# Optimization experiments

Hardware: AMD Instinct MI355X
Metric: run time of the kernel (lower is better)

The kernel has to match this reference:

```python
import jax, jax.numpy as jnp
import numpy as np

L, B, H, S, V, D = 2, 128, 1024, 512, 32000, 64
W_SCALE = 0.02

def setup_inputs() -> dict:
    key = jax.random.key(0)
    ks = jax.random.split(key, 17)
    f = lambda k, shape: jax.random.normal(k, shape, dtype=jnp.float32)
    return {
        "input_ids": jax.random.randint(ks[0], (1, B), 0, V),
        "h": f(ks[1], (L, B, H)),
        "c": f(ks[2], (L, B, H)),
        "h_s": f(ks[3], (S, B, H)),
        "emb": f(ks[4], (V, H)),
        "W_pt": f(ks[5], (H, H)) * W_SCALE,
        "b_pt": f(ks[6], (H,)) * W_SCALE,
        "v_pt": f(ks[7], (H,)) * W_SCALE,
        "b_v": f(ks[8], (1,)) * W_SCALE,
        "W_a": f(ks[9], (H, H)) * W_SCALE,
        "b_a": f(ks[10], (1,)) * W_SCALE,
        "W_ih": f(ks[11], (L, 4 * H, H)) * W_SCALE,
        "W_hh": f(ks[12], (L, 4 * H, H)) * W_SCALE,
        "b_ih": f(ks[13], (L, 4 * H)) * W_SCALE,
        "b_hh": f(ks[14], (L, 4 * H)) * W_SCALE,
        "W_out": f(ks[15], (V, H)) * W_SCALE,
        "b_out": f(ks[16], (V,)) * W_SCALE,
    }


def reference(input_ids, h, c, h_s, emb, W_pt, b_pt, v_pt, b_v, W_a, b_a,
              W_ih, W_hh, b_ih, b_hh, W_out, b_out):
    S_len = h_s.shape[0]
    x_emb = emb[input_ids]                     # [1, B, H]
    h_top = h[-1]                              # [B, H] top-layer decoder state
    # predicted alignment position p_t = S * sigmoid(v . tanh(W h + b))
    p_t = S_len * jax.nn.sigmoid(jnp.tanh(h_top @ W_pt.T + b_pt) @ v_pt + b_v[0])  # [B]
    s = jnp.clip(jnp.round(p_t).astype(jnp.int32), D, S_len - 1 - D)               # [B]
    # gather local window h_s[s-D : s+D+1] per batch element
    idx = s[:, None] + jnp.arange(-D, D + 1)    # [B, 2D+1]
    h_s_b = jnp.transpose(h_s, (1, 0, 2))       # [B, S, H]
    h_loc = jnp.take_along_axis(h_s_b, idx[:, :, None], axis=1)  # [B, 2D+1, H]
    # bilinear score h_t^T W_a h_s_j per window position
    scores = jnp.einsum('bh,hk,bjk->bj', h_top, W_a, h_loc) + b_a[0]  # [B, 2D+1]
    sigma2 = (D / 2.0) ** 2
    gauss = jnp.exp(-((idx.astype(p_t.dtype) - p_t[:, None]) ** 2) / (2.0 * sigma2))
    a_t = jax.nn.softmax(scores, axis=-1) * gauss                      # [B, 2D+1]
    context = jnp.einsum('bj,bjh->bh', a_t, h_loc)                     # [B, H]
    # inject context into the LSTM hidden state, then run one step
    h_in = h + context[None]                    # [L, B, H]
    x = x_emb[0]                                # [B, H]
    hs, cs = [], []
    for l in range(h.shape[0]):
        gates = x @ W_ih[l].T + b_ih[l] + h_in[l] @ W_hh[l].T + b_hh[l]
        i, f, g, o = jnp.split(gates, 4, axis=-1)
        c_new = jax.nn.sigmoid(f) * c[l] + jax.nn.sigmoid(i) * jnp.tanh(g)
        h_new = jax.nn.sigmoid(o) * jnp.tanh(c_new)
        hs.append(h_new)
        cs.append(c_new)
        x = h_new
    h_out = jnp.stack(hs)                       # [L, B, H]
    c_out = jnp.stack(cs)                       # [L, B, H]
    logits = jax.nn.log_softmax(x @ W_out.T + b_out, axis=-1)  # [B, V]
    return logits, h_out, c_out, context, s
```

## Files before the change

kernel.cpp:

```cpp
#include <hip/hip_runtime.h>
#include <hip/hip_bf16.h>
#include <math.h>

typedef __bf16 bf16_8 __attribute__((ext_vector_type(8)));
typedef __bf16 bf16_4 __attribute__((ext_vector_type(4)));
typedef float  f32x4  __attribute__((ext_vector_type(4)));

static __device__ __forceinline__ float sigmoidf_(float x){ return 1.0f/(1.0f + expf(-x)); }

#define BB 128
#define HH 1024
#define SS 512
#define VV 32000

#define OFF_A0    0u
#define OFF_A1    524288u
#define OFF_ALOG  1048576u
#define OFF_AH    1310720u
#define OFF_AM    1572864u
#define OFF_AL    1835008u
#define OFF_WAT   2097152u
#define OFF_Q     6291456u
#define OFF_Z     6815744u
#define OFF_PT    7340032u
#define OFF_SI    7340544u
#define OFF_SC    7341056u
#define OFF_AT    7408640u
#define OFF_G0    7476224u
#define OFF_G1    9573376u
#define OFF_PMAX  11670528u
#define OFF_PSUM  11801600u
#define OFF_LSE   11932672u

__global__ void k_transpose(const float* __restrict__ in, float* __restrict__ out){
  __shared__ float t[32][33];
  int kt = blockIdx.x, nt = blockIdx.y;
  int c = threadIdx.x & 31, r0 = threadIdx.x >> 5;
  #pragma unroll
  for (int i = 0; i < 4; ++i){
    int r = r0 + 8*i;
    t[r][c] = in[(size_t)(kt*32 + r)*HH + nt*32 + c];
  }
  __syncthreads();
  #pragma unroll
  for (int i = 0; i < 4; ++i){
    int r = r0 + 8*i;
    out[(size_t)(nt*32 + r)*HH + kt*32 + c] = t[c][r];
  }
}

__global__ void k_prep(const int* __restrict__ ids, const float* __restrict__ emb,
                       const float* __restrict__ h,
                       const float* __restrict__ b_pt,
                       const float* __restrict__ b_ih, const float* __restrict__ b_hh,
                       __bf16* __restrict__ A0, __bf16* __restrict__ Ah,
                       __bf16* __restrict__ Am, __bf16* __restrict__ Al,
                       float* __restrict__ z, float* __restrict__ q,
                       float* __restrict__ g0, float* __restrict__ g1){
  int blk = blockIdx.x, t = threadIdx.x;
  if (blk < BB){
    int b = blk, c = t*4;
    int tok = ids[b];
    f32x4 e = *(const f32x4*)(emb + (size_t)tok*HH + c);
    bf16_4 e4;
    #pragma unroll
    for (int i=0;i<4;i++) e4[i] = (__bf16)e[i];
    *(bf16_4*)(A0 + (size_t)b*2048 + c) = e4;
    f32x4 x = *(const f32x4*)(h + (size_t)BB*HH + (size_t)b*HH + c);
    bf16_4 hi4, mi4, lo4;
    #pragma unroll
    for (int i=0;i<4;i++){
      float v = x[i];
      __bf16 bh = (__bf16)v; float r1 = v - (float)bh;
      __bf16 bm = (__bf16)r1; float r2 = r1 - (float)bm;
      hi4[i]=bh; mi4[i]=bm; lo4[i]=(__bf16)r2;
    }
    *(bf16_4*)(Ah + (size_t)b*HH + c) = hi4;
    *(bf16_4*)(Am + (size_t)b*HH + c) = mi4;
    *(bf16_4*)(Al + (size_t)b*HH + c) = lo4;
    *(f32x4*)(z + (size_t)b*HH + c) = *(const f32x4*)(b_pt + c);
    *(f32x4*)(q + (size_t)b*HH + c) = f32x4{0.f,0.f,0.f,0.f};
  } else {
    int b = blk - BB;
    for (int i=t; i<4096; i+=256){
      g0[(size_t)b*4096 + i] = b_ih[i] + b_hh[i];
      g1[(size_t)b*4096 + i] = b_ih[4096+i] + b_hh[4096+i];
    }
  }
}

template<int PREC, int EPI>
__global__ __launch_bounds__(256) void k_gemm(
    const __bf16* __restrict__ Ah, const __bf16* __restrict__ Am, const __bf16* __restrict__ Al,
    int lda,
    const float* __restrict__ B1, const float* __restrict__ B2, int K1, int K2,
    const float* __restrict__ bias,
    float* __restrict__ C, int N,
    float* __restrict__ Pmax, float* __restrict__ Psum)
{
  constexpr int NS  = PREC;
  constexpr int BK  = (PREC == 1) ? 64 : 32;
  constexpr int KG  = BK/8;
  constexpr int TILE = 128*BK*2;
  constexpr int UPT = (128*KG)/256;
  __shared__ __align__(16) char smem[NS*2*TILE];
  char* sA = smem;
  char* sB = smem + NS*TILE;

  const int t = threadIdx.x;
  const int lane = t & 63, wave = t >> 6;
  const int wm = wave >> 1, wn = wave & 1;
  const int quad = lane >> 4, ln = lane & 15;
  const int nblock = blockIdx.x * 128;
  const int K = K1 + K2;
  const int kchunk = K / gridDim.y;
  const int kstart = blockIdx.y * kchunk;
  const int kend = kstart + kchunk;

  f32x4 acc[4][4];
  #pragma unroll
  for (int i=0;i<4;i++)
    #pragma unroll
    for (int j=0;j<4;j++) acc[i][j] = f32x4{0.f,0.f,0.f,0.f};

  if constexpr (PREC == 1){
    uint4 aR[UPT]; f32x4 bR[UPT][2];
    auto issue = [&](int k0){
      #pragma unroll
      for (int i=0;i<UPT;++i){
        int u = t + 256*i, row = u/KG, kg = u%KG;
        aR[i] = *(const uint4*)(Ah + (size_t)row*lda + k0 + kg*8);
        int ng = nblock + row;
        const float* src = (k0 < K1) ? (B1 + (size_t)ng*K1 + k0 + kg*8)
                                     : (B2 + (size_t)ng*K2 + (k0 - K1) + kg*8);
        bR[i][0] = *(const f32x4*)(src);
        bR[i][1] = *(const f32x4*)(src + 4);
      }
    };
    issue(kstart);
    for (int k0 = kstart; k0 < kend; k0 += BK){
      __syncthreads();
      #pragma unroll
      for (int i=0;i<UPT;++i){
        int u = t + 256*i, row = u/KG, kg = u%KG;
        int sl = row*(BK*2) + (((kg ^ (row & (KG-1)))) << 4);
        *(uint4*)(sA + sl) = aR[i];
        bf16_8 hi;
        #pragma unroll
        for (int q=0;q<8;++q) hi[q] = (__bf16)((q<4) ? bR[i][0][q] : bR[i][1][q-4]);
        *(bf16_8*)(sB + sl) = hi;
      }
      __syncthreads();
      if (k0 + BK < kend) issue(k0 + BK);
      #pragma unroll
      for (int ks = 0; ks < BK/32; ++ks){
        bf16_8 af[4], bfr[4];
        #pragma unroll
        for (int mt=0; mt<4; ++mt){
          int row = wm*64 + mt*16 + ln;
          int kg = ks*4 + quad;
          int sl = row*(BK*2) + (((kg ^ (row & (KG-1)))) << 4);
          af[mt] = *(const bf16_8*)(sA + sl);
        }
        #pragma unroll
        for (int nt=0; nt<4; ++nt){
          int row = wn*64 + nt*16 + ln;
          int kg = ks*4 + quad;
          int sl = row*(BK*2) + (((kg ^ (row & (KG-1)))) << 4);
          bfr[nt] = *(const bf16_8*)(sB + sl);
        }
        #pragma unroll
        for (int mt=0; mt<4; ++mt)
          #pragma unroll
          for (int nt=0; nt<4; ++nt)
            acc[mt][nt] = __builtin_amdgcn_mfma_f32_16x16x32_bf16(af[mt], bfr[nt], acc[mt][nt], 0,0,0);
      }
    }
  } else {
    for (int k0 = kstart; k0 < kend; k0 += BK){
      #pragma unroll
      for (int i = 0; i < UPT; ++i){
        int u = t + 256*i;
        int row = u / KG, kg = u % KG;
        int sl = row*(BK*2) + (((kg ^ (row & (KG-1)))) << 4);
        *(uint4*)(sA + sl) = *(const uint4*)(Ah + (size_t)row*lda + k0 + kg*8);
        if constexpr (PREC >= 2)
          *(uint4*)(sA + TILE + sl) = *(const uint4*)(Am + (size_t)row*lda + k0 + kg*8);
        if constexpr (PREC >= 3)
          *(uint4*)(sA + 2*TILE + sl) = *(const uint4*)(Al + (size_t)row*lda + k0 + kg*8);
        int ng = nblock + row;
        const float* src = B1 + (size_t)ng*K1 + k0 + kg*8;
        f32x4 x0 = *(const f32x4*)(src);
        f32x4 x1 = *(const f32x4*)(src + 4);
        bf16_8 hi, mi, lo;
        #pragma unroll
        for (int q=0;q<8;q++){
          float v = (q<4) ? x0[q] : x1[q-4];
          __bf16 bh = (__bf16)v;
          hi[q] = bh;
          float r1 = v - (float)bh;
          __bf16 bm = (__bf16)r1;
          mi[q] = bm;
          lo[q] = (__bf16)(r1 - (float)bm);
        }
        *(bf16_8*)(sB + sl) = hi;
        if constexpr (PREC >= 2) *(bf16_8*)(sB + TILE + sl) = mi;
        if constexpr (PREC >= 3) *(bf16_8*)(sB + 2*TILE + sl) = lo;
      }
      __syncthreads();
      #pragma unroll
      for (int ks = 0; ks < BK/32; ++ks){
        bf16_8 af[NS][4], bfr[NS][4];
        #pragma unroll
        for (int mt=0; mt<4; ++mt){
          int row = wm*64 + mt*16 + ln;
          int kg = ks*4 + quad;
          int sl = row*(BK*2) + (((kg ^ (row & (KG-1)))) << 4);
          #pragma unroll
          for (int s=0;s<NS;s++) af[s][mt] = *(const bf16_8*)(sA + s*TILE + sl);
        }
        #pragma unroll
        for (int nt=0; nt<4; ++nt){
          int row = wn*64 + nt*16 + ln;
          int kg = ks*4 + quad;
          int sl = row*(BK*2) + (((kg ^ (row & (KG-1)))) << 4);
          #pragma unroll
          for (int s=0;s<NS;s++) bfr[s][nt] = *(const bf16_8*)(sB + s*TILE + sl);
        }
        #pragma unroll
        for (int mt=0; mt<4; ++mt)
          #pragma unroll
          for (int nt=0; nt<4; ++nt){
            acc[mt][nt] = __builtin_amdgcn_mfma_f32_16x16x32_bf16(af[0][mt], bfr[0][nt], acc[mt][nt], 0,0,0);
            if constexpr (PREC >= 2){
              acc[mt][nt] = __builtin_amdgcn_mfma_f32_16x16x32_bf16(af[0][mt], bfr[1][nt], acc[mt][nt], 0,0,0);
              acc[mt][nt] = __builtin_amdgcn_mfma_f32_16x16x32_bf16(af[1][mt], bfr[0][nt], acc[mt][nt], 0,0,0);
            }
            if constexpr (PREC >= 3){
              acc[mt][nt] = __builtin_amdgcn_mfma_f32_16x16x32_bf16(af[0][mt], bfr[2][nt], acc[mt][nt], 0,0,0);
              acc[mt][nt] = __builtin_amdgcn_mfma_f32_16x16x32_bf16(af[1][mt], bfr[1][nt], acc[mt][nt], 0,0,0);
              acc[mt][nt] = __builtin_amdgcn_mfma_f32_16x16x32_bf16(af[2][mt], bfr[0][nt], acc[mt][nt], 0,0,0);
            }
          }
      }
      __syncthreads();
    }
  }

  if constexpr (EPI == 0){
    #pragma unroll
    for (int nt=0; nt<4; ++nt){
      int n = nblock + wn*64 + nt*16 + ln;
      float bv = bias ? bias[n] : 0.f;
      #pragma unroll
      for (int mt=0; mt<4; ++mt){
        int m0 = wm*64 + mt*16 + quad*4;
        #pragma unroll
        for (int r=0;r<4;++r)
          C[(size_t)(m0 + r)*N + n] = acc[mt][nt][r] + bv;
      }
    }
  } else if constexpr (EPI == 3){
    #pragma unroll
    for (int nt=0; nt<4; ++nt){
      int n = nblock + wn*64 + nt*16 + ln;
      #pragma unroll
      for (int mt=0; mt<4; ++mt){
        int m0 = wm*64 + mt*16 + quad*4;
        #pragma unroll
        for (int r=0;r<4;++r)
          atomicAdd(C + (size_t)(m0 + r)*N + n, acc[mt][nt][r]);
      }
    }
  } else if constexpr (EPI == 2){
    __syncthreads();
    float* redm = (float*)smem;
    float* reds = (float*)smem + 256;
    float rmax[16];
    #pragma unroll
    for (int mt=0; mt<4; ++mt)
      #pragma unroll
      for (int r=0;r<4;++r){
        float m4 = -1e30f;
        #pragma unroll
        for (int nt=0;nt<4;++nt){
          int n = nblock + wn*64 + nt*16 + ln;
          m4 = fmaxf(m4, acc[mt][nt][r] + bias[n]);
        }
        #pragma unroll
        for (int m=1;m<16;m<<=1) m4 = fmaxf(m4, __shfl_xor(m4, m));
        rmax[mt*4+r] = m4;
      }
    if (ln == 0){
      #pragma unroll
      for (int mt=0;mt<4;++mt)
        #pragma unroll
        for (int r=0;r<4;++r)
          redm[wn*128 + wm*64 + mt*16 + quad*4 + r] = rmax[mt*4+r];
    }
    __syncthreads();
    #pragma unroll
    for (int mt=0; mt<4; ++mt)
      #pragma unroll
      for (int r=0;r<4;++r){
        int row = wm*64 + mt*16 + quad*4 + r;
        float M = fmaxf(redm[row], redm[128 + row]);
        float s4 = 0.f;
        #pragma unroll
        for (int nt=0;nt<4;++nt){
          int n = nblock + wn*64 + nt*16 + ln;
          float v = acc[mt][nt][r] + bias[n];
          C[(size_t)row*N + n] = v;
          s4 += expf(v - M);
        }
        #pragma unroll
        for (int m=1;m<16;m<<=1) s4 += __shfl_xor(s4, m);
        if (ln == 0) reds[wn*128 + row] = s4;
      }
    __syncthreads();
    if (wn == 0 && ln == 0){
      #pragma unroll
      for (int mt=0;mt<4;++mt)
        #pragma unroll
        for (int r=0;r<4;++r){
          int row = wm*64 + mt*16 + quad*4 + r;
          float M = fmaxf(redm[row], redm[128 + row]);
          Pmax[(size_t)blockIdx.x*128 + row] = M;
          Psum[(size_t)blockIdx.x*128 + row] = reds[row] + reds[128 + row];
        }
    }
  }
}

__global__ void k_s2(const float* __restrict__ z, const float* __restrict__ v_pt,
                     const float* __restrict__ b_v,
                     float* __restrict__ p_t, int* __restrict__ s_i, float* __restrict__ out_s){
  __shared__ float red[4];
  int b = blockIdx.x, t = threadIdx.x;
  f32x4 zv = *(const f32x4*)(z + (size_t)b*HH + t*4);
  f32x4 vv = *(const f32x4*)(v_pt + t*4);
  float s = tanhf(zv[0])*vv[0] + tanhf(zv[1])*vv[1] + tanhf(zv[2])*vv[2] + tanhf(zv[3])*vv[3];
  #pragma unroll
  for (int m=1;m<64;m<<=1) s += __shfl_xor(s, m);
  if ((t&63)==0) red[t>>6] = s;
  __syncthreads();
  if (t == 0){
    float tot = red[0]+red[1]+red[2]+red[3] + b_v[0];
    float p = (float)SS * sigmoidf_(tot);
    float sf = rintf(p);
    sf = fminf(fmaxf(sf, 64.0f), 447.0f);
    p_t[b] = p; s_i[b] = (int)sf; out_s[b] = sf;
  }
}

__global__ void k_scores(const float* __restrict__ q, const float* __restrict__ h_s,
                         const int* __restrict__ s_i, const float* __restrict__ b_a,
                         float* __restrict__ sc){
  int b = blockIdx.x;
  int jj = blockIdx.y*4 + (threadIdx.x >> 6);
  if (jj >= 129) return;
  int lane = threadIdx.x & 63;
  int pos = s_i[b] - 64 + jj;
  const float* row = h_s + ((size_t)pos*BB + b)*HH;
  const float* qb  = q + (size_t)b*HH;
  f32x4 a = f32x4{0.f,0.f,0.f,0.f};
  #pragma unroll
  for (int c = lane*4; c < HH; c += 256){
    f32x4 r4 = *(const f32x4*)(row + c);
    f32x4 q4 = *(const f32x4*)(qb + c);
    a += r4*q4;
  }
  float s = a[0]+a[1]+a[2]+a[3];
  #pragma unroll
  for (int m=1;m<64;m<<=1) s += __shfl_xor(s, m);
  if (lane == 0) sc[b*132 + jj] = s + b_a[0];
}

__global__ void k_softmax(const float* __restrict__ sc, const int* __restrict__ s_i,
                          const float* __restrict__ p_t, float* __restrict__ a_t){
  int b = blockIdx.x, l = threadIdx.x;
  const float* scb = sc + b*132;
  float mx = -1e30f;
  for (int j=l; j<129; j+=64) mx = fmaxf(mx, scb[j]);
  #pragma unroll
  for (int m=1;m<64;m<<=1) mx = fmaxf(mx, __shfl_xor(mx, m));
  float sum = 0.f;
  for (int j=l; j<129; j+=64) sum += expf(scb[j] - mx);
  #pragma unroll
  for (int m=1;m<64;m<<=1) sum += __shfl_xor(sum, m);
  float inv = 1.0f/sum;
  float pt = p_t[b]; float s0 = (float)(s_i[b] - 64);
  for (int j=l; j<129; j+=64){
    float e = expf(scb[j]-mx)*inv;
    float d = (s0 + (float)j) - pt;
    a_t[b*132 + j] = e * expf(-(d*d) * (1.0f/2048.0f));
  }
}

__global__ __launch_bounds__(256) void k_context(
    const float* __restrict__ a_t, const float* __restrict__ h_s,
    const int* __restrict__ s_i, const float* __restrict__ h,
    float* __restrict__ ctx_out, __bf16* __restrict__ A0, __bf16* __restrict__ A1){
  __shared__ float sat[132];
  __shared__ float sctx[4][1024];
  int b = blockIdx.x, t = threadIdx.x;
  int w = t >> 6, l = t & 63;
  if (t < 129) sat[t] = a_t[b*132 + t];
  __syncthreads();
  int pos0 = s_i[b] - 64;
  int jstart = (w == 0) ? 0 : (33 + 32*(w-1));
  int jcnt   = (w == 0) ? 33 : 32;
  const float* base = h_s + ((size_t)pos0*BB + b)*HH;
  f32x4 acc[4];
  #pragma unroll
  for (int qq=0;qq<4;++qq) acc[qq] = f32x4{0.f,0.f,0.f,0.f};
  for (int j = jstart; j < jstart + jcnt; ++j){
    const float* row = base + (size_t)j*BB*HH;
    float aj = sat[j];
    #pragma unroll
    for (int qq=0;qq<4;++qq){
      f32x4 r = *(const f32x4*)(row + qq*256 + l*4);
      acc[qq] += r * aj;
    }
  }
  #pragma unroll
  for (int qq=0;qq<4;++qq)
    *(f32x4*)(&sctx[w][qq*256 + l*4]) = acc[qq];
  __syncthreads();
  int c = t*4;
  f32x4 v = *(f32x4*)(&sctx[0][c]) + *(f32x4*)(&sctx[1][c])
          + *(f32x4*)(&sctx[2][c]) + *(f32x4*)(&sctx[3][c]);
  *(f32x4*)(ctx_out + (size_t)b*HH + c) = v;
  f32x4 h0 = *(const f32x4*)(h + (size_t)b*HH + c) + v;
  f32x4 h1 = *(const f32x4*)(h + (size_t)BB*HH + (size_t)b*HH + c) + v;
  bf16_4 v0, v1;
  #pragma unroll
  for (int i=0;i<4;i++){ v0[i]=(__bf16)h0[i]; v1[i]=(__bf16)h1[i]; }
  *(bf16_4*)(A0 + (size_t)b*2048 + 1024 + c) = v0;
  *(bf16_4*)(A1 + (size_t)b*2048 + 1024 + c) = v1;
}

__global__ void k_cell(const float* __restrict__ gates, const float* __restrict__ c_in,
                       float* __restrict__ h_out, float* __restrict__ c_out,
                       __bf16* __restrict__ Anext, int strideNext){
  int g = blockIdx.x*256 + threadIdx.x;
  int b = g >> 10, hc = g & 1023;
  const float* gb = gates + (size_t)b*4096;
  float ig = gb[hc], fg = gb[1024+hc], gg = gb[2048+hc], og = gb[3072+hc];
  float cn = sigmoidf_(fg)*c_in[g] + sigmoidf_(ig)*tanhf(gg);
  float hn = sigmoidf_(og)*tanhf(cn);
  c_out[g] = cn; h_out[g] = hn;
  Anext[(size_t)b*strideNext + hc] = (__bf16)hn;
}

__global__ void k_lse2(const float* __restrict__ Pmax, const float* __restrict__ Psum,
                       float* __restrict__ lse){
  int b = blockIdx.x, l = threadIdx.x;
  float M = -1e30f;
  for (int i=l; i<250; i+=64) M = fmaxf(M, Pmax[(size_t)i*128 + b]);
  #pragma unroll
  for (int m=1;m<64;m<<=1) M = fmaxf(M, __shfl_xor(M, m));
  float s = 0.f;
  for (int i=l; i<250; i+=64) s += Psum[(size_t)i*128 + b] * expf(Pmax[(size_t)i*128 + b] - M);
  #pragma unroll
  for (int m=1;m<64;m<<=1) s += __shfl_xor(s, m);
  if (l == 0) lse[b] = M + logf(s);
}

__global__ void k_sub(float* __restrict__ out, const float* __restrict__ lse){
  int b = blockIdx.y;
  int i = blockIdx.x*256 + threadIdx.x*4;
  float L = lse[b];
  f32x4 v = *(f32x4*)(out + (size_t)b*VV + i);
  v[0]-=L; v[1]-=L; v[2]-=L; v[3]-=L;
  *(f32x4*)(out + (size_t)b*VV + i) = v;
}

extern "C" void kernel_launch(void* const* d_in, const int* in_sizes, int n_in,
                              void* d_out, int out_size, void* d_ws, size_t ws_size,
                              hipStream_t stream){
  const int*   ids   = (const int*)d_in[0];
  const float* h     = (const float*)d_in[1];
  const float* c     = (const float*)d_in[2];
  const float* h_s   = (const float*)d_in[3];
  const float* emb   = (const float*)d_in[4];
  const float* W_pt  = (const float*)d_in[5];
  const float* b_pt  = (const float*)d_in[6];
  const float* v_pt  = (const float*)d_in[7];
  const float* b_v   = (const float*)d_in[8];
  const float* W_a   = (const float*)d_in[9];
  const float* b_a   = (const float*)d_in[10];
  const float* W_ih  = (const float*)d_in[11];
  const float* W_hh  = (const float*)d_in[12];
  const float* b_ih  = (const float*)d_in[13];
  const float* b_hh  = (const float*)d_in[14];
  const float* W_out = (const float*)d_in[15];
  const float* b_out = (const float*)d_in[16];

  char* ws = (char*)d_ws;
  __bf16* A0   = (__bf16*)(ws + OFF_A0);
  __bf16* A1   = (__bf16*)(ws + OFF_A1);
  __bf16* Alog = (__bf16*)(ws + OFF_ALOG);
  __bf16* Ah   = (__bf16*)(ws + OFF_AH);
  __bf16* Am   = (__bf16*)(ws + OFF_AM);
  __bf16* Al   = (__bf16*)(ws + OFF_AL);
  float* WaT   = (float*)(ws + OFF_WAT);
  float* q     = (float*)(ws + OFF_Q);
  float* z     = (float*)(ws + OFF_Z);
  float* p_t   = (float*)(ws + OFF_PT);
  int*   s_i   = (int*)  (ws + OFF_SI);
  float* sc    = (float*)(ws + OFF_SC);
  float* a_t   = (float*)(ws + OFF_AT);
  float* g0    = (float*)(ws + OFF_G0);
  float* g1    = (float*)(ws + OFF_G1);
  float* Pmax  = (float*)(ws + OFF_PMAX);
  float* Psum  = (float*)(ws + OFF_PSUM);
  float* lse   = (float*)(ws + OFF_LSE);

  float* out        = (float*)d_out;
  float* out_logits = out;
  float* out_h      = out + 4096000;
  float* out_c      = out + 4358144;
  float* out_ctx    = out + 4620288;
  float* out_s      = out + 4751360;

  k_transpose<<<dim3(32,32), 256, 0, stream>>>(W_a, WaT);
  k_prep<<<256, 256, 0, stream>>>(ids, emb, h, b_pt, b_ih, b_hh, A0, Ah, Am, Al, z, q, g0, g1);
  k_gemm<2,3><<<dim3(8,4), 256, 0, stream>>>(Ah, Am, nullptr, 1024, WaT, nullptr, 1024, 0,
                                             nullptr, q, 1024, nullptr, nullptr);
  k_gemm<3,3><<<dim3(8,4), 256, 0, stream>>>(Ah, Am, Al, 1024, W_pt, nullptr, 1024, 0,
                                             nullptr, z, 1024, nullptr, nullptr);
  k_s2<<<128, 256, 0, stream>>>(z, v_pt, b_v, p_t, s_i, out_s);
  k_scores<<<dim3(128, 33), 256, 0, stream>>>(q, h_s, s_i, b_a, sc);
  k_softmax<<<128, 64, 0, stream>>>(sc, s_i, p_t, a_t);
  k_context<<<128, 256, 0, stream>>>(a_t, h_s, s_i, h, out_ctx, A0, A1);
  k_gemm<1,3><<<dim3(32,4), 256, 0, stream>>>(A0, nullptr, nullptr, 2048, W_ih, W_hh, 1024, 1024,
                                              nullptr, g0, 4096, nullptr, nullptr);
  k_cell<<<512, 256, 0, stream>>>(g0, c, out_h, out_c, A1, 2048);
  k_gemm<1,3><<<dim3(32,4), 256, 0, stream>>>(A1, nullptr, nullptr, 2048, W_ih + 4194304, W_hh + 4194304,
                                              1024, 1024, nullptr, g1, 4096, nullptr, nullptr);
  k_cell<<<512, 256, 0, stream>>>(g1, c + 131072, out_h + 131072, out_c + 131072, Alog, 1024);
  k_gemm<1,2><<<dim3(250,1), 256, 0, stream>>>(Alog, nullptr, nullptr, 1024, W_out, nullptr, 1024, 0,
                                               b_out, out_logits, 32000, Pmax, Psum);
  k_lse2<<<128, 64, 0, stream>>>(Pmax, Psum, lse);
  k_sub<<<dim3(125,128), 64, 0, stream>>>(out_logits, lse);
}
```

Before: 653.1 us.

## Fuse attention and LSTM pipeline kernels, replace atomics with split-K partial buffers

Merges the W_a transpose and the prep work into one launch, and runs the q and z small GEMMs together in one kernel. The p_t/s computation moves into the scores kernel, and the softmax plus gaussian weighting moves into the context kernel, which now splits each batch row across two blocks. The LSTM gate GEMMs write split-K partials to separate buffers instead of using atomicAdd; the cell kernel sums the four partials and adds the biases. LSE reduction and subtraction become one kernel. This cuts launch count, bias-init traffic and atomic contention, but adds recomputation of p_t in every score block and of LSE in every subtract block, plus extra partial-buffer traffic.

```diff
diff --git a/kernel.cpp b/kernel.cpp
--- a/kernel.cpp
+++ b/kernel.cpp
@@ -25,41 +25,35 @@
 #define OFF_PT    7340032u
 #define OFF_SI    7340544u
 #define OFF_SC    7341056u
-#define OFF_AT    7408640u
-#define OFF_G0    7476224u
-#define OFF_G1    9573376u
-#define OFF_PMAX  11670528u
-#define OFF_PSUM  11801600u
-#define OFF_LSE   11932672u
-
-__global__ void k_transpose(const float* __restrict__ in, float* __restrict__ out){
-  __shared__ float t[32][33];
-  int kt = blockIdx.x, nt = blockIdx.y;
-  int c = threadIdx.x & 31, r0 = threadIdx.x >> 5;
-  #pragma unroll
-  for (int i = 0; i < 4; ++i){
-    int r = r0 + 8*i;
-    t[r][c] = in[(size_t)(kt*32 + r)*HH + nt*32 + c];
-  }
-  __syncthreads();
-  #pragma unroll
-  for (int i = 0; i < 4; ++i){
-    int r = r0 + 8*i;
-    out[(size_t)(nt*32 + r)*HH + kt*32 + c] = t[c][r];
-  }
-}
-
-__global__ void k_prep(const int* __restrict__ ids, const float* __restrict__ emb,
-                       const float* __restrict__ h,
-                       const float* __restrict__ b_pt,
-                       const float* __restrict__ b_ih, const float* __restrict__ b_hh,
-                       __bf16* __restrict__ A0, __bf16* __restrict__ Ah,
-                       __bf16* __restrict__ Am, __bf16* __restrict__ Al,
-                       float* __restrict__ z, float* __restrict__ q,
-                       float* __restrict__ g0, float* __restrict__ g1){
+#define OFF_G0P   7408640u
+#define OFF_G1P   15797248u
+#define OFF_PMAX  24185856u
+#define OFF_PSUM  24313856u
+
+__global__ void k_prep_all(const float* __restrict__ W_a, float* __restrict__ WaT,
+                           const int* __restrict__ ids, const float* __restrict__ emb,
+                           const float* __restrict__ h, const float* __restrict__ b_pt,
+                           __bf16* __restrict__ A0, __bf16* __restrict__ Ah,
+                           __bf16* __restrict__ Am, __bf16* __restrict__ Al,
+                           float* __restrict__ z, float* __restrict__ q){
+  __shared__ float tsm[32][33];
   int blk = blockIdx.x, t = threadIdx.x;
-  if (blk < BB){
-    int b = blk, c = t*4;
+  if (blk < 1024){
+    int kt = blk & 31, nt = blk >> 5;
+    int c = t & 31, r0 = t >> 5;
+    #pragma unroll
+    for (int i = 0; i < 4; ++i){
+      int r = r0 + 8*i;
+      tsm[r][c] = W_a[(size_t)(kt*32 + r)*HH + nt*32 + c];
+    }
+    __syncthreads();
+    #pragma unroll
+    for (int i = 0; i < 4; ++i){
+      int r = r0 + 8*i;
+      WaT[(size_t)(nt*32 + r)*HH + kt*32 + c] = tsm[c][r];
+    }
+  } else {
+    int b = blk - 1024, c = t*4;
     int tok = ids[b];
     f32x4 e = *(const f32x4*)(emb + (size_t)tok*HH + c);
     bf16_4 e4;
@@ -80,13 +74,130 @@
     *(bf16_4*)(Al + (size_t)b*HH + c) = lo4;
     *(f32x4*)(z + (size_t)b*HH + c) = *(const f32x4*)(b_pt + c);
     *(f32x4*)(q + (size_t)b*HH + c) = f32x4{0.f,0.f,0.f,0.f};
-  } else {
-    int b = blk - BB;
-    for (int i=t; i<4096; i+=256){
-      g0[(size_t)b*4096 + i] = b_ih[i] + b_hh[i];
-      g1[(size_t)b*4096 + i] = b_ih[4096+i] + b_hh[4096+i];
-    }
-  }
+  }
+}
+
+template<int PREC>
+__device__ __forceinline__ void gemm_small(
+    char* smem,
+    const __bf16* __restrict__ Ah, const __bf16* __restrict__ Am, const __bf16* __restrict__ Al,
+    int lda, const float* __restrict__ B1, int K,
+    float* __restrict__ C, int N, int xblk, int ysplit)
+{
+  constexpr int NS   = PREC;
+  constexpr int BK   = 32;
+  constexpr int KG   = BK/8;
+  constexpr int TILE = 128*BK*2;
+  constexpr int UPT  = (128*KG)/256;
+  char* sA = smem;
+  char* sB = smem + NS*TILE;
+
+  const int t = threadIdx.x;
+  const int lane = t & 63, wave = t >> 6;
+  const int wm = wave >> 1, wn = wave & 1;
+  const int quad = lane >> 4, ln = lane & 15;
+  const int nblock = xblk * 128;
+  const int kchunk = K / ysplit;
+  const int kstart = blockIdx.y * kchunk;
+  const int kend = kstart + kchunk;
+
+  f32x4 acc[4][4];
+  #pragma unroll
+  for (int i=0;i<4;i++)
+    #pragma unroll
+    for (int j=0;j<4;j++) acc[i][j] = f32x4{0.f,0.f,0.f,0.f};
+
+  for (int k0 = kstart; k0 < kend; k0 += BK){
+    #pragma unroll
+    for (int i = 0; i < UPT; ++i){
+      int u = t + 256*i;
+      int row = u / KG, kg = u % KG;
+      int sl = row*(BK*2) + (((kg ^ (row & (KG-1)))) << 4);
+      *(uint4*)(sA + sl) = *(const uint4*)(Ah + (size_t)row*lda + k0 + kg*8);
+      if constexpr (PREC >= 2)
+        *(uint4*)(sA + TILE + sl) = *(const uint4*)(Am + (size_t)row*lda + k0 + kg*8);
+      if constexpr (PREC >= 3)
+        *(uint4*)(sA + 2*TILE + sl) = *(const uint4*)(Al + (size_t)row*lda + k0 + kg*8);
+      int ng = nblock + row;
+      const float* src = B1 + (size_t)ng*K + k0 + kg*8;
+      f32x4 x0 = *(const f32x4*)(src);
+      f32x4 x1 = *(const f32x4*)(src + 4);
+      bf16_8 hi, mi, lo;
+      #pragma unroll
+      for (int qv=0;qv<8;qv++){
+        float v = (qv<4) ? x0[qv] : x1[qv-4];
+        __bf16 bh = (__bf16)v;
+        hi[qv] = bh;
+        float r1 = v - (float)bh;
+        __bf16 bm = (__bf16)r1;
+        mi[qv] = bm;
+        lo[qv] = (__bf16)(r1 - (float)bm);
+      }
+      *(bf16_8*)(sB + sl) = hi;
+      if constexpr (PREC >= 2) *(bf16_8*)(sB + TILE + sl) = mi;
+      if constexpr (PREC >= 3) *(bf16_8*)(sB + 2*TILE + sl) = lo;
+    }
+    __syncthreads();
+    {
+      bf16_8 af[NS][4], bfr[NS][4];
+      #pragma unroll
+      for (int mt=0; mt<4; ++mt){
+        int row = wm*64 + mt*16 + ln;
+        int kg = quad;
+        int sl = row*(BK*2) + (((kg ^ (row & (KG-1)))) << 4);
+        #pragma unroll
+        for (int s=0;s<NS;s++) af[s][mt] = *(const bf16_8*)(sA + s*TILE + sl);
+      }
+      #pragma unroll
+      for (int nt=0; nt<4; ++nt){
+        int row = wn*64 + nt*16 + ln;
+        int kg = quad;
+        int sl = row*(BK*2) + (((kg ^ (row & (KG-1)))) << 4);
+        #pragma unroll
+        for (int s=0;s<NS;s++) bfr[s][nt] = *(const bf16_8*)(sB + s*TILE + sl);
+      }
+      #pragma unroll
+      for (int mt=0; mt<4; ++mt)
+        #pragma unroll
+        for (int nt=0; nt<4; ++nt){
+          acc[mt][nt] = __builtin_amdgcn_mfma_f32_16x16x32_bf16(af[0][mt], bfr[0][nt], acc[mt][nt], 0,0,0);
+          if constexpr (PREC >= 2){
+            acc[mt][nt] = __builtin_amdgcn_mfma_f32_16x16x32_bf16(af[0][mt], bfr[1][nt], acc[mt][nt], 0,0,0);
+            acc[mt][nt] = __builtin_amdgcn_mfma_f32_16x16x32_bf16(af[1][mt], bfr[0][nt], acc[mt][nt], 0,0,0);
+          }
+          if constexpr (PREC >= 3){
+            acc[mt][nt] = __builtin_amdgcn_mfma_f32_16x16x32_bf16(af[0][mt], bfr[2][nt], acc[mt][nt], 0,0,0);
+            acc[mt][nt] = __builtin_amdgcn_mfma_f32_16x16x32_bf16(af[1][mt], bfr[1][nt], acc[mt][nt], 0,0,0);
+            acc[mt][nt] = __builtin_amdgcn_mfma_f32_16x16x32_bf16(af[2][mt], bfr[0][nt], acc[mt][nt], 0,0,0);
+          }
+        }
+    }
+    __syncthreads();
+  }
+
+  #pragma unroll
+  for (int nt=0; nt<4; ++nt){
+    int n = nblock + wn*64 + nt*16 + ln;
+    #pragma unroll
+    for (int mt=0; mt<4; ++mt){
+      int m0 = wm*64 + mt*16 + quad*4;
+      #pragma unroll
+      for (int r=0;r<4;++r)
+        atomicAdd(C + (size_t)(m0 + r)*N + n, acc[mt][nt][r]);
+    }
+  }
+}
+
+__global__ __launch_bounds__(256) void k_qz(
+    const __bf16* __restrict__ Ah, const __bf16* __restrict__ Am, const __bf16* __restrict__ Al,
+    const float* __restrict__ WaT, const float* __restrict__ Wpt,
+    float* __restrict__ q, float* __restrict__ z)
+{
+  __shared__ __align__(16) char smem[49152];
+  if (blockIdx.x < 8)
+    gemm_small<2>(smem, Ah, Am, nullptr, 1024, WaT, 1024, q, 1024, blockIdx.x, 4);
+  else
+    gemm_small<3>(smem, Ah, Am, Al, 1024, Wpt, 1024, z, 1024, blockIdx.x - 8, 4);
 }
 
 template<int PREC, int EPI>
@@ -98,14 +209,13 @@
     float* __restrict__ C, int N,
     float* __restrict__ Pmax, float* __restrict__ Psum)
 {
-  constexpr int NS  = PREC;
-  constexpr int BK  = (PREC == 1) ? 64 : 32;
+  constexpr int BK  = 64;
   constexpr int KG  = BK/8;
   constexpr int TILE = 128*BK*2;
   constexpr int UPT = (128*KG)/256;
-  __shared__ __align__(16) char smem[NS*2*TILE];
+  __shared__ __align__(16) char smem[2*TILE];
   char* sA = smem;
-  char* sB = smem + NS*TILE;
+  char* sB = smem + TILE;
 
   const int t = threadIdx.x;
   const int lane = t & 63, wave = t >> 6;
@@ -123,153 +233,70 @@
     #pragma unroll
     for (int j=0;j<4;j++) acc[i][j] = f32x4{0.f,0.f,0.f,0.f};
 
-  if constexpr (PREC == 1){
-    uint4 aR[UPT]; f32x4 bR[UPT][2];
-    auto issue = [&](int k0){
-      #pragma unroll
-      for (int i=0;i<UPT;++i){
-        int u = t + 256*i, row = u/KG, kg = u%KG;
-        aR[i] = *(const uint4*)(Ah + (size_t)row*lda + k0 + kg*8);
-        int ng = nblock + row;
-        const float* src = (k0 < K1) ? (B1 + (size_t)ng*K1 + k0 + kg*8)
-                                     : (B2 + (size_t)ng*K2 + (k0 - K1) + kg*8);
-        bR[i][0] = *(const f32x4*)(src);
-        bR[i][1] = *(const f32x4*)(src + 4);
-      }
-    };
-    issue(kstart);
-    for (int k0 = kstart; k0 < kend; k0 += BK){
-      __syncthreads();
-      #pragma unroll
-      for (int i=0;i<UPT;++i){
-        int u = t + 256*i, row = u/KG, kg = u%KG;
+  uint4 aR[UPT]; f32x4 bR[UPT][2];
+  auto issue = [&](int k0){
+    #pragma unroll
+    for (int i=0;i<UPT;++i){
+      int u = t + 256*i, row = u/KG, kg = u%KG;
+      aR[i] = *(const uint4*)(Ah + (size_t)row*lda + k0 + kg*8);
+      int ng = nblock + row;
+      const float* src = (k0 < K1) ? (B1 + (size_t)ng*K1 + k0 + kg*8)
+                                   : (B2 + (size_t)ng*K2 + (k0 - K1) + kg*8);
+      bR[i][0] = *(const f32x4*)(src);
+      bR[i][1] = *(const f32x4*)(src + 4);
+    }
+  };
+  issue(kstart);
+  for (int k0 = kstart; k0 < kend; k0 += BK){
+    __syncthreads();
+    #pragma unroll
+    for (int i=0;i<UPT;++i){
+      int u = t + 256*i, row = u/KG, kg = u%KG;
+      int sl = row*(BK*2) + (((kg ^ (row & (KG-1)))) << 4);
+      *(uint4*)(sA + sl) = aR[i];
+      bf16_8 hi;
+      #pragma unroll
+      for (int qv=0;qv<8;++qv) hi[qv] = (__bf16)((qv<4) ? bR[i][0][qv] : bR[i][1][qv-4]);
+      *(bf16_8*)(sB + sl) = hi;
+    }
+    __syncthreads();
+    if (k0 + BK < kend) issue(k0 + BK);
+    #pragma unroll
+    for (int ks = 0; ks < BK/32; ++ks){
+      bf16_8 af[4], bfr[4];
+      #pragma unroll
+      for (int mt=0; mt<4; ++mt){
+        int row = wm*64 + mt*16 + ln;
+        int kg = ks*4 + quad;
         int sl = row*(BK*2) + (((kg ^ (row & (KG-1)))) << 4);
-        *(uint4*)(sA + sl) = aR[i];
-        bf16_8 hi;
-        #pragma unroll
-        for (int q=0;q<8;++q) hi[q] = (__bf16)((q<4) ? bR[i][0][q] : bR[i][1][q-4]);
-        *(bf16_8*)(sB + sl) = hi;
-      }
-      __syncthreads();
-      if (k0 + BK < kend) issue(k0 + BK);
-      #pragma unroll
-      for (int ks = 0; ks < BK/32; ++ks){
-        bf16_8 af[4], bfr[4];
-        #pragma unroll
-        for (int mt=0; mt<4; ++mt){
-          int row = wm*64 + mt*16 + ln;
-          int kg = ks*4 + quad;
-          int sl = row*(BK*2) + (((kg ^ (row & (KG-1)))) << 4);
-          af[mt] = *(const bf16_8*)(sA + sl);
-        }
-        #pragma unroll
-        for (int nt=0; nt<4; ++nt){
-          int row = wn*64 + nt*16 + ln;
-          int kg = ks*4 + quad;
-          int sl = row*(BK*2) + (((kg ^ (row & (KG-1)))) << 4);
-          bfr[nt] = *(const bf16_8*)(sB + sl);
-        }
-        #pragma unroll
-        for (int mt=0; mt<4; ++mt)
-          #pragma unroll
-          for (int nt=0; nt<4; ++nt)
-            acc[mt][nt] = __builtin_amdgcn_mfma_f32_16x16x32_bf16(af[mt], bfr[nt], acc[mt][nt], 0,0,0);
-      }
-    }
-  } else {
-    for (int k0 = kstart; k0 < kend; k0 += BK){
-      #pragma unroll
-      for (int i = 0; i < UPT; ++i){
-        int u = t + 256*i;
-        int row = u / KG, kg = u % KG;
+        af[mt] = *(const bf16_8*)(sA + sl);
+      }
+      #pragma unroll
+      for (int nt=0; nt<4; ++nt){
+        int row = wn*64 + nt*16 + ln;
+        int kg = ks*4 + quad;
         int sl = row*(BK*2) + (((kg ^ (row & (KG-1)))) << 4);
-        *(uint4*)(sA + sl) = *(const uint4*)(Ah + (size_t)row*lda + k0 + kg*8);
-        if constexpr (PREC >= 2)
-          *(uint4*)(sA + TILE + sl) = *(const uint4*)(Am + (size_t)row*lda + k0 + kg*8);
-        if constexpr (PREC >= 3)
-          *(uint4*)(sA + 2*TILE + sl) = *(const uint4*)(Al + (size_t)row*lda + k0 + kg*8);
-        int ng = nblock + row;
-        const float* src = B1 + (size_t)ng*K1 + k0 + kg*8;
-        f32x4 x0 = *(const f32x4*)(src);
-        f32x4 x1 = *(const f32x4*)(src + 4);
-        bf16_8 hi, mi, lo;
-        #pragma unroll
-        for (int q=0;q<8;q++){
-          float v = (q<4) ? x0[q] : x1[q-4];
-          __bf16 bh = (__bf16)v;
-          hi[q] = bh;
-          float r1 = v - (float)bh;
-          __bf16 bm = (__bf16)r1;
-          mi[q] = bm;
-          lo[q] = (__bf16)(r1 - (float)bm);
-        }
-        *(bf16_8*)(sB + sl) = hi;
-        if constexpr (PREC >= 2) *(bf16_8*)(sB + TILE + sl) = mi;
-        if constexpr (PREC >= 3) *(bf16_8*)(sB + 2*TILE + sl) = lo;
-      }
-      __syncthreads();
-      #pragma unroll
-      for (int ks = 0; ks < BK/32; ++ks){
-        bf16_8 af[NS][4], bfr[NS][4];
-        #pragma unroll
-        for (int mt=0; mt<4; ++mt){
-          int row = wm*64 + mt*16 + ln;
-          int kg = ks*4 + quad;
-          int sl = row*(BK*2) + (((kg ^ (row & (KG-1)))) << 4);
-          #pragma unroll
-          for (int s=0;s<NS;s++) af[s][mt] = *(const bf16_8*)(sA + s*TILE + sl);
-        }
-        #pragma unroll
-        for (int nt=0; nt<4; ++nt){
-          int row = wn*64 + nt*16 + ln;
-          int kg = ks*4 + quad;
-          int sl = row*(BK*2) + (((kg ^ (row & (KG-1)))) << 4);
-          #pragma unroll
-          for (int s=0;s<NS;s++) bfr[s][nt] = *(const bf16_8*)(sB + s*TILE + sl);
-        }
-        #pragma unroll
-        for (int mt=0; mt<4; ++mt)
-          #pragma unroll
-          for (int nt=0; nt<4; ++nt){
-            acc[mt][nt] = __builtin_amdgcn_mfma_f32_16x16x32_bf16(af[0][mt], bfr[0][nt], acc[mt][nt], 0,0,0);
-            if constexpr (PREC >= 2){
-              acc[mt][nt] = __builtin_amdgcn_mfma_f32_16x16x32_bf16(af[0][mt], bfr[1][nt], acc[mt][nt], 0,0,0);
-              acc[mt][nt] = __builtin_amdgcn_mfma_f32_16x16x32_bf16(af[1][mt], bfr[0][nt], acc[mt][nt], 0,0,0);
-            }
-            if constexpr (PREC >= 3){
-              acc[mt][nt] = __builtin_amdgcn_mfma_f32_16x16x32_bf16(af[0][mt], bfr[2][nt], acc[mt][nt], 0,0,0);
-              acc[mt][nt] = __builtin_amdgcn_mfma_f32_16x16x32_bf16(af[1][mt], bfr[1][nt], acc[mt][nt], 0,0,0);
-              acc[mt][nt] = __builtin_amdgcn_mfma_f32_16x16x32_bf16(af[2][mt], bfr[0][nt], acc[mt][nt], 0,0,0);
-            }
-          }
-      }
-      __syncthreads();
-    }
-  }
-
-  if constexpr (EPI == 0){
+        bfr[nt] = *(const bf16_8*)(sB + sl);
+      }
+      #pragma unroll
+      for (int mt=0; mt<4; ++mt)
+        #pragma unroll
+        for (int nt=0; nt<4; ++nt)
+          acc[mt][nt] = __builtin_amdgcn_mfma_f32_16x16x32_bf16(af[mt], bfr[nt], acc[mt][nt], 0,0,0);
+    }
+  }
+
+  if constexpr (EPI == 4){
+    float* Cp = C + (size_t)blockIdx.y * 128 * N;
     #pragma unroll
     for (int nt=0; nt<4; ++nt){
       int n = nblock + wn*64 + nt*16 + ln;
-      float bv = bias ? bias[n] : 0.f;
       #pragma unroll
       for (int mt=0; mt<4; ++mt){
         int m0 = wm*64 + mt*16 + quad*4;
         #pragma unroll
         for (int r=0;r<4;++r)
-          C[(size_t)(m0 + r)*N + n] = acc[mt][nt][r] + bv;
-      }
-    }
-  } else if constexpr (EPI == 3){
-    #pragma unroll
-    for (int nt=0; nt<4; ++nt){
-      int n = nblock + wn*64 + nt*16 + ln;
-      #pragma unroll
-      for (int mt=0; mt<4; ++mt){
-        int m0 = wm*64 + mt*16 + quad*4;
-        #pragma unroll
-        for (int r=0;r<4;++r)
-          atomicAdd(C + (size_t)(m0 + r)*N + n, acc[mt][nt][r]);
+          Cp[(size_t)(m0 + r)*N + n] = acc[mt][nt][r];
       }
     }
   } else if constexpr (EPI == 2){
@@ -332,35 +359,39 @@
   }
 }
 
-__global__ void k_s2(const float* __restrict__ z, const float* __restrict__ v_pt,
-                     const float* __restrict__ b_v,
-                     float* __restrict__ p_t, int* __restrict__ s_i, float* __restrict__ out_s){
+__global__ __launch_bounds__(256) void k_scores(
+    const float* __restrict__ z, const float* __restrict__ v_pt, const float* __restrict__ b_v,
+    const float* __restrict__ q, const float* __restrict__ h_s,
+    const float* __restrict__ b_a,
+    float* __restrict__ sc, float* __restrict__ p_t, int* __restrict__ s_i,
+    float* __restrict__ out_s)
+{
   __shared__ float red[4];
+  __shared__ float sh[2];
   int b = blockIdx.x, t = threadIdx.x;
-  f32x4 zv = *(const f32x4*)(z + (size_t)b*HH + t*4);
-  f32x4 vv = *(const f32x4*)(v_pt + t*4);
-  float s = tanhf(zv[0])*vv[0] + tanhf(zv[1])*vv[1] + tanhf(zv[2])*vv[2] + tanhf(zv[3])*vv[3];
-  #pragma unroll
-  for (int m=1;m<64;m<<=1) s += __shfl_xor(s, m);
-  if ((t&63)==0) red[t>>6] = s;
-  __syncthreads();
-  if (t == 0){
-    float tot = red[0]+red[1]+red[2]+red[3] + b_v[0];
-    float p = (float)SS * sigmoidf_(tot);
-    float sf = rintf(p);
-    sf = fminf(fmaxf(sf, 64.0f), 447.0f);
-    p_t[b] = p; s_i[b] = (int)sf; out_s[b] = sf;
-  }
-}
-
-__global__ void k_scores(const float* __restrict__ q, const float* __restrict__ h_s,
-                         const int* __restrict__ s_i, const float* __restrict__ b_a,
-                         float* __restrict__ sc){
-  int b = blockIdx.x;
-  int jj = blockIdx.y*4 + (threadIdx.x >> 6);
+  {
+    f32x4 zv = *(const f32x4*)(z + (size_t)b*HH + t*4);
+    f32x4 vv = *(const f32x4*)(v_pt + t*4);
+    float ps = tanhf(zv[0])*vv[0] + tanhf(zv[1])*vv[1] + tanhf(zv[2])*vv[2] + tanhf(zv[3])*vv[3];
+    #pragma unroll
+    for (int m=1;m<64;m<<=1) ps += __shfl_xor(ps, m);
+    if ((t&63)==0) red[t>>6] = ps;
+    __syncthreads();
+    if (t == 0){
+      float tot = red[0]+red[1]+red[2]+red[3] + b_v[0];
+      float p = (float)SS * sigmoidf_(tot);
+      float sf = rintf(p);
+      sf = fminf(fmaxf(sf, 64.0f), 447.0f);
+      sh[0] = p; sh[1] = sf;
+      if (blockIdx.y == 0){ p_t[b] = p; s_i[b] = (int)sf; out_s[b] = sf; }
+    }
+    __syncthreads();
+  }
+  int si = (int)sh[1];
+  int jj = blockIdx.y*4 + (t >> 6);
   if (jj >= 129) return;
-  int lane = threadIdx.x & 63;
-  int pos = s_i[b] - 64 + jj;
+  int lane = t & 63;
+  int pos = si - 64 + jj;
   const float* row = h_s + ((size_t)pos*BB + b)*HH;
   const float* qb  = q + (size_t)b*HH;
   f32x4 a = f32x4{0.f,0.f,0.f,0.f};
@@ -370,92 +401,100 @@
     f32x4 q4 = *(const f32x4*)(qb + c);
     a += r4*q4;
   }
-  float s = a[0]+a[1]+a[2]+a[3];
-  #pragma unroll
-  for (int m=1;m<64;m<<=1) s += __shfl_xor(s, m);
-  if (lane == 0) sc[b*132 + jj] = s + b_a[0];
-}
-
-__global__ void k_softmax(const float* __restrict__ sc, const int* __restrict__ s_i,
-                          const float* __restrict__ p_t, float* __restrict__ a_t){
-  int b = blockIdx.x, l = threadIdx.x;
-  const float* scb = sc + b*132;
-  float mx = -1e30f;
-  for (int j=l; j<129; j+=64) mx = fmaxf(mx, scb[j]);
-  #pragma unroll
-  for (int m=1;m<64;m<<=1) mx = fmaxf(mx, __shfl_xor(mx, m));
-  float sum = 0.f;
-  for (int j=l; j<129; j+=64) sum += expf(scb[j] - mx);
-  #pragma unroll
-  for (int m=1;m<64;m<<=1) sum += __shfl_xor(sum, m);
-  float inv = 1.0f/sum;
-  float pt = p_t[b]; float s0 = (float)(s_i[b] - 64);
-  for (int j=l; j<129; j+=64){
-    float e = expf(scb[j]-mx)*inv;
-    float d = (s0 + (float)j) - pt;
-    a_t[b*132 + j] = e * expf(-(d*d) * (1.0f/2048.0f));
-  }
+  float sdot = a[0]+a[1]+a[2]+a[3];
+  #pragma unroll
+  for (int m=1;m<64;m<<=1) sdot += __shfl_xor(sdot, m);
+  if (lane == 0) sc[b*132 + jj] = sdot + b_a[0];
 }
 
 __global__ __launch_bounds__(256) void k_context(
-    const float* __restrict__ a_t, const float* __restrict__ h_s,
-    const int* __restrict__ s_i, const float* __restrict__ h,
+    const float* __restrict__ sc, const int* __restrict__ s_i, const float* __restrict__ p_t,
+    const float* __restrict__ h_s, const float* __restrict__ h,
     float* __restrict__ ctx_out, __bf16* __restrict__ A0, __bf16* __restrict__ A1){
   __shared__ float sat[132];
-  __shared__ float sctx[4][1024];
-  int b = blockIdx.x, t = threadIdx.x;
-  int w = t >> 6, l = t & 63;
-  if (t < 129) sat[t] = a_t[b*132 + t];
+  __shared__ float sctx[4][512];
+  __shared__ int spos;
+  int bb = blockIdx.x;
+  int b = bb >> 1, half = bb & 1;
+  int t = threadIdx.x, w = t >> 6, l = t & 63;
+  if (w == 0){
+    const float* scb = sc + b*132;
+    float mx = -1e30f;
+    for (int j=l; j<129; j+=64) mx = fmaxf(mx, scb[j]);
+    #pragma unroll
+    for (int m=1;m<64;m<<=1) mx = fmaxf(mx, __shfl_xor(mx, m));
+    float sum = 0.f;
+    for (int j=l; j<129; j+=64) sum += expf(scb[j] - mx);
+    #pragma unroll
+    for (int m=1;m<64;m<<=1) sum += __shfl_xor(sum, m);
+    float inv = 1.0f/sum;
+    float pt = p_t[b];
+    int si = s_i[b];
+    if (l == 0) spos = si - 64;
+    float s0 = (float)(si - 64);
+    for (int j=l; j<129; j+=64){
+      float e = expf(scb[j]-mx)*inv;
+      float d = (s0 + (float)j) - pt;
+      sat[j] = e * expf(-(d*d) * (1.0f/2048.0f));
+    }
+  }
   __syncthreads();
-  int pos0 = s_i[b] - 64;
+  int pos0 = spos;
   int jstart = (w == 0) ? 0 : (33 + 32*(w-1));
   int jcnt   = (w == 0) ? 33 : 32;
-  const float* base = h_s + ((size_t)pos0*BB + b)*HH;
-  f32x4 acc[4];
-  #pragma unroll
-  for (int qq=0;qq<4;++qq) acc[qq] = f32x4{0.f,0.f,0.f,0.f};
+  const float* base = h_s + ((size_t)pos0*BB + b)*HH + half*512;
+  f32x4 acc0 = f32x4{0.f,0.f,0.f,0.f};
+  f32x4 acc1 = f32x4{0.f,0.f,0.f,0.f};
   for (int j = jstart; j < jstart + jcnt; ++j){
     const float* row = base + (size_t)j*BB*HH;
     float aj = sat[j];
-    #pragma unroll
-    for (int qq=0;qq<4;++qq){
-      f32x4 r = *(const f32x4*)(row + qq*256 + l*4);
-      acc[qq] += r * aj;
-    }
-  }
-  #pragma unroll
-  for (int qq=0;qq<4;++qq)
-    *(f32x4*)(&sctx[w][qq*256 + l*4]) = acc[qq];
+    acc0 += *(const f32x4*)(row + l*4) * aj;
+    acc1 += *(const f32x4*)(row + 256 + l*4) * aj;
+  }
+  *(f32x4*)(&sctx[w][l*4])       = acc0;
+  *(f32x4*)(&sctx[w][256 + l*4]) = acc1;
   __syncthreads();
-  int c = t*4;
-  f32x4 v = *(f32x4*)(&sctx[0][c]) + *(f32x4*)(&sctx[1][c])
-          + *(f32x4*)(&sctx[2][c]) + *(f32x4*)(&sctx[3][c]);
-  *(f32x4*)(ctx_out + (size_t)b*HH + c) = v;
-  f32x4 h0 = *(const f32x4*)(h + (size_t)b*HH + c) + v;
-  f32x4 h1 = *(const f32x4*)(h + (size_t)BB*HH + (size_t)b*HH + c) + v;
-  bf16_4 v0, v1;
-  #pragma unroll
-  for (int i=0;i<4;i++){ v0[i]=(__bf16)h0[i]; v1[i]=(__bf16)h1[i]; }
-  *(bf16_4*)(A0 + (size_t)b*2048 + 1024 + c) = v0;
-  *(bf16_4*)(A1 + (size_t)b*2048 + 1024 + c) = v1;
-}
-
-__global__ void k_cell(const float* __restrict__ gates, const float* __restrict__ c_in,
+  if (t < 128){
+    int c = t*4;
+    f32x4 v = *(f32x4*)(&sctx[0][c]) + *(f32x4*)(&sctx[1][c])
+            + *(f32x4*)(&sctx[2][c]) + *(f32x4*)(&sctx[3][c]);
+    int gc = half*512 + c;
+    *(f32x4*)(ctx_out + (size_t)b*HH + gc) = v;
+    f32x4 h0 = *(const f32x4*)(h + (size_t)b*HH + gc) + v;
+    f32x4 h1 = *(const f32x4*)(h + (size_t)BB*HH + (size_t)b*HH + gc) + v;
+    bf16_4 v0, v1;
+    #pragma unroll
+    for (int i=0;i<4;i++){ v0[i]=(__bf16)h0[i]; v1[i]=(__bf16)h1[i]; }
+    *(bf16_4*)(A0 + (size_t)b*2048 + 1024 + gc) = v0;
+    *(bf16_4*)(A1 + (size_t)b*2048 + 1024 + gc) = v1;
+  }
+}
+
+__global__ void k_cell(const float* __restrict__ part,
+                       const float* __restrict__ bih, const float* __restrict__ bhh,
+                       const float* __restrict__ c_in,
                        float* __restrict__ h_out, float* __restrict__ c_out,
                        __bf16* __restrict__ Anext, int strideNext){
   int g = blockIdx.x*256 + threadIdx.x;
   int b = g >> 10, hc = g & 1023;
-  const float* gb = gates + (size_t)b*4096;
-  float ig = gb[hc], fg = gb[1024+hc], gg = gb[2048+hc], og = gb[3072+hc];
+  float ig = bih[hc]        + bhh[hc];
+  float fg = bih[1024 + hc] + bhh[1024 + hc];
+  float gg = bih[2048 + hc] + bhh[2048 + hc];
+  float og = bih[3072 + hc] + bhh[3072 + hc];
+  #pragma unroll
+  for (int y = 0; y < 4; ++y){
+    const float* gb = part + ((size_t)y*BB + b)*4096;
+    ig += gb[hc]; fg += gb[1024+hc]; gg += gb[2048+hc]; og += gb[3072+hc];
+  }
   float cn = sigmoidf_(fg)*c_in[g] + sigmoidf_(ig)*tanhf(gg);
   float hn = sigmoidf_(og)*tanhf(cn);
   c_out[g] = cn; h_out[g] = hn;
   Anext[(size_t)b*strideNext + hc] = (__bf16)hn;
 }
 
-__global__ void k_lse2(const float* __restrict__ Pmax, const float* __restrict__ Psum,
-                       float* __restrict__ lse){
-  int b = blockIdx.x, l = threadIdx.x;
+__global__ void k_lsesub(const float* __restrict__ Pmax, const float* __restrict__ Psum,
+                         float* __restrict__ out){
+  int b = blockIdx.y, l = threadIdx.x;
   float M = -1e30f;
   for (int i=l; i<250; i+=64) M = fmaxf(M, Pmax[(size_t)i*128 + b]);
   #pragma unroll
@@ -464,13 +503,8 @@
   for (int i=l; i<250; i+=64) s += Psum[(size_t)i*128 + b] * expf(Pmax[(size_t)i*128 + b] - M);
   #pragma unroll
   for (int m=1;m<64;m<<=1) s += __shfl_xor(s, m);
-  if (l == 0) lse[b] = M + logf(s);
-}
-
-__global__ void k_sub(float* __restrict__ out, const float* __restrict__ lse){
-  int b = blockIdx.y;
-  int i = blockIdx.x*256 + threadIdx.x*4;
-  float L = lse[b];
+  float L = M + logf(s);
+  int i = blockIdx.x*256 + l*4;
   f32x4 v = *(f32x4*)(out + (size_t)b*VV + i);
   v[0]-=L; v[1]-=L; v[2]-=L; v[3]-=L;
   *(f32x4*)(out + (size_t)b*VV + i) = v;
@@ -510,12 +544,10 @@
   float* p_t   = (float*)(ws + OFF_PT);
   int*   s_i   = (int*)  (ws + OFF_SI);
   float* sc    = (float*)(ws + OFF_SC);
-  float* a_t   = (float*)(ws + OFF_AT);
-  float* g0    = (float*)(ws + OFF_G0);
-  float* g1    = (float*)(ws + OFF_G1);
+  float* g0p   = (float*)(ws + OFF_G0P);
+  float* g1p   = (float*)(ws + OFF_G1P);
   float* Pmax  = (float*)(ws + OFF_PMAX);
   float* Psum  = (float*)(ws + OFF_PSUM);
-  float* lse   = (float*)(ws + OFF_LSE);
 
   float* out        = (float*)d_out;
   float* out_logits = out;
@@ -524,24 +556,18 @@
   float* out_ctx    = out + 4620288;
   float* out_s      = out + 4751360;
 
-  k_transpose<<<dim3(32,32), 256, 0, stream>>>(W_a, WaT);
-  k_prep<<<256, 256, 0, stream>>>(ids, emb, h, b_pt, b_ih, b_hh, A0, Ah, Am, Al, z, q, g0, g1);
-  k_gemm<2,3><<<dim3(8,4), 256, 0, stream>>>(Ah, Am, nullptr, 1024, WaT, nullptr, 1024, 0,
-                                             nullptr, q, 1024, nullptr, nullptr);
-  k_gemm<3,3><<<dim3(8,4), 256, 0, stream>>>(Ah, Am, Al, 1024, W_pt, nullptr, 1024, 0,
-                                             nullptr, z, 1024, nullptr, nullptr);
-  k_s2<<<128, 256, 0, stream>>>(z, v_pt, b_v, p_t, s_i, out_s);
-  k_scores<<<dim3(128, 33), 256, 0, stream>>>(q, h_s, s_i, b_a, sc);
-  k_softmax<<<128, 64, 0, stream>>>(sc, s_i, p_t, a_t);
-  k_context<<<128, 256, 0, stream>>>(a_t, h_s, s_i, h, out_ctx, A0, A1);
-  k_gemm<1,3><<<dim3(32,4), 256, 0, stream>>>(A0, nullptr, nullptr, 2048, W_ih, W_hh, 1024, 1024,
-                                              nullptr, g0, 4096, nullptr, nullptr);
-  k_cell<<<512, 256, 0, stream>>>(g0, c, out_h, out_c, A1, 2048);
-  k_gemm<1,3><<<dim3(32,4), 256, 0, stream>>>(A1, nullptr, nullptr, 2048, W_ih + 4194304, W_hh + 4194304,
-                                              1024, 1024, nullptr, g1, 4096, nullptr, nullptr);
-  k_cell<<<512, 256, 0, stream>>>(g1, c + 131072, out_h + 131072, out_c + 131072, Alog, 1024);
+  k_prep_all<<<1152, 256, 0, stream>>>(W_a, WaT, ids, emb, h, b_pt, A0, Ah, Am, Al, z, q);
+  k_qz<<<dim3(16,4), 256, 0, stream>>>(Ah, Am, Al, WaT, W_pt, q, z);
+  k_scores<<<dim3(128,33), 256, 0, stream>>>(z, v_pt, b_v, q, h_s, b_a, sc, p_t, s_i, out_s);
+  k_context<<<256, 256, 0, stream>>>(sc, s_i, p_t, h_s, h, out_ctx, A0, A1);
+  k_gemm<1,4><<<dim3(32,4), 256, 0, stream>>>(A0, nullptr, nullptr, 2048, W_ih, W_hh, 1024, 1024,
+                                              nullptr, g0p, 4096, nullptr, nullptr);
+  k_cell<<<512, 256, 0, stream>>>(g0p, b_ih, b_hh, c, out_h, out_c, A1, 2048);
+  k_gemm<1,4><<<dim3(32,4), 256, 0, stream>>>(A1, nullptr, nullptr, 2048, W_ih + 4194304, W_hh + 4194304,
+                                              1024, 1024, nullptr, g1p, 4096, nullptr, nullptr);
+  k_cell<<<512, 256, 0, stream>>>(g1p, b_ih + 4096, b_hh + 4096, c + 131072,
+                                  out_h + 131072, out_c + 131072, Alog, 1024);
   k_gemm<1,2><<<dim3(250,1), 256, 0, stream>>>(Alog, nullptr, nullptr, 1024, W_out, nullptr, 1024, 0,
                                                b_out, out_logits, 32000, Pmax, Psum);
-  k_lse2<<<128, 64, 0, stream>>>(Pmax, Psum, lse);
-  k_sub<<<dim3(125,128), 64, 0, stream>>>(out_logits, lse);
-}
+  k_lsesub<<<dim3(125,128), 64, 0, stream>>>(Pmax, Psum, out_logits);
+}
```

Measured after the change: 651.5 us. About the same (-0.3%).
